# Performance work log

Hardware: AMD Instinct MI355X
Metric: run time of the kernel (lower is better)

Reference implementation:

```python
import jax, jax.numpy as jnp
import numpy as np
import math

D_MODEL, N_HEADS, BATCH, SEQ = 1024, 16, 2, 2048
D_HEAD = D_MODEL // N_HEADS


def setup_inputs() -> dict:
    key = jax.random.key(0)
    ks = jax.random.split(key, 5)
    w = lambda k: jax.random.normal(k, (D_MODEL, D_MODEL), jnp.float32) * 0.02
    return {
        "X": jax.random.normal(ks[0], (BATCH, SEQ, D_MODEL), jnp.float32),
        "W_q": w(ks[1]),
        "W_k": w(ks[2]),
        "W_v": w(ks[3]),
        "W_o": w(ks[4]),
        "g_q": jnp.ones((D_MODEL,), jnp.float32),
        "b_q": jnp.zeros((D_MODEL,), jnp.float32),
        "g_k": jnp.ones((D_MODEL,), jnp.float32),
        "b_k": jnp.zeros((D_MODEL,), jnp.float32),
        "cache_k": jnp.zeros((BATCH, N_HEADS, SEQ, D_HEAD), jnp.float32),
        "cache_v": jnp.zeros((BATCH, N_HEADS, SEQ, D_HEAD), jnp.float32),
        "start_pos": 0,
    }


def _layernorm(x, g, b, eps=1e-5):
    mu = jnp.mean(x, axis=-1, keepdims=True)
    xc = x - mu
    var = jnp.mean(xc * xc, axis=-1, keepdims=True)
    return xc * jax.lax.rsqrt(var + eps) * g + b


def reference(X, W_q, W_k, W_v, W_o, g_q, b_q, g_k, b_k, cache_k, cache_v, start_pos):
    batch, N, d_model = X.shape
    H = cache_k.shape[1]
    dh = d_model // H

    # QK-normed projections (torch Linear: x @ W^T)
    XQ = _layernorm(X @ W_q.T, g_q, b_q)
    XK = _layernorm(X @ W_k.T, g_k, b_k)
    XV = X @ W_v.T
    split = lambda t: t.reshape(batch, N, H, dh).transpose(0, 2, 1, 3)  # [b,h,n,d]
    XQ, XK, XV = split(XQ), split(XK), split(XV)

    # KV-cache scatter update, then slice to valid prefix (start_pos is static)
    cache_k = jax.lax.dynamic_update_slice(cache_k, XK, (0, 0, start_pos, 0))
    cache_v = jax.lax.dynamic_update_slice(cache_v, XV, (0, 0, start_pos, 0))
    M = start_pos + N
    K = cache_k[:, :, :M]
    V = cache_v[:, :, :M]

    logits = jnp.einsum('bhnd,bhmd->bhnm', XQ, K) / math.sqrt(dh)  # [b,h,N,M]

    # causal mask on the freshly written block [start_pos:M]
    tril = jnp.tril(jnp.ones((N, N), bool))
    full_mask = jnp.concatenate([jnp.ones((N, start_pos), bool), tril], axis=1)  # [N,M]
    logits = jnp.where(full_mask[None, None], logits, -jnp.inf)

    # selective forget-mask bias built from relu'd head-0 logits
    S = jax.nn.relu(logits[:, 0])               # relu(-inf) -> 0, matches torch
    S = S.at[..., 0].set(0.0)                   # zero first column
    S = S * (1.0 - jnp.eye(N, dtype=S.dtype))   # zero diagonal (valid since start_pos==0)
    S = jnp.roll(S, 1, axis=-2)                 # shift rows down by one
    S = S.at[..., 0, :].set(0.0)
    F_mask = jnp.cumsum(S, axis=-2)             # [b,N,M]

    logits = logits - F_mask[:, None]
    attn = jax.nn.softmax(logits, axis=-1)
    O = jnp.einsum('bhnm,bhmd->bhnd', attn, V)
    O = O.transpose(0, 2, 1, 3).reshape(batch, N, d_model)
    return O @ W_o.T
```

## Files before the change

kernel.cpp:

```cpp
#include <hip/hip_runtime.h>
#include <cstdint>
#include <cstddef>


typedef unsigned short u16;
typedef __attribute__((ext_vector_type(8))) __bf16 bf16x8;
typedef __attribute__((ext_vector_type(4))) float f32x4;
typedef __attribute__((ext_vector_type(2))) unsigned int uint2v;

#define D_MODEL 1024
#define N_HEADS 16
#define BATCH   2
#define SEQ     2048
#define D_HEAD  64
#define ROWS    (BATCH*SEQ)
#define NSEG    64
#define SEGLEN  32
#define LOG2E   1.44269504f

static __device__ __forceinline__ u16 f2bf(float f){
  union { float f; uint32_t u; } v; v.f = f;
  uint32_t r = v.u + 0x7fffu + ((v.u >> 16) & 1u);
  return (u16)(r >> 16);
}
static __device__ __forceinline__ float bf2f(u16 h){
  union { uint32_t u; float f; } v; v.u = ((uint32_t)h) << 16;
  return v.f;
}
static __device__ __forceinline__ uint32_t cvtpk(float lo, float hi){
  uint32_t r;
  asm("v_cvt_pk_bf16_f32 %0, %1, %2" : "=v"(r) : "v"(lo), "v"(hi));
  return r;
}
#define GLDS(gp, lp) __builtin_amdgcn_global_load_lds( \
    (const __attribute__((address_space(1))) void*)(gp), \
    (__attribute__((address_space(3))) void*)(lp), 16, 0, 0)

__global__ void k_cast_all(const float* __restrict__ X,
                           u16* __restrict__ Xhi, u16* __restrict__ Xlo,
                           const float* __restrict__ Wq,
                           u16* __restrict__ Wqh, u16* __restrict__ Wql,
                           const float* __restrict__ Wk,
                           u16* __restrict__ Wkh, u16* __restrict__ Wkl,
                           const float* __restrict__ Wv, u16* __restrict__ Wvb,
                           const float* __restrict__ Wo, u16* __restrict__ Wob){
  int i = blockIdx.x*256 + threadIdx.x;
  if (i < 1572864){
    const float* src; u16 *dh, *dl; int base;
    if (i < 1048576){ src = X;  dh = Xhi; dl = Xlo; base = i; }
    else if (i < 1310720){ src = Wq; dh = Wqh; dl = Wql; base = i - 1048576; }
    else { src = Wk; dh = Wkh; dl = Wkl; base = i - 1310720; }
    float4 v = reinterpret_cast<const float4*>(src)[base];
    float vs[4] = {v.x, v.y, v.z, v.w};
    union { u16 s[4]; uint2 u; } uh, ul;
#pragma unroll
    for (int r=0;r<4;++r){
      uh.s[r] = f2bf(vs[r]);
      ul.s[r] = f2bf(vs[r] - bf2f(uh.s[r]));
    }
    reinterpret_cast<uint2*>(dh)[base] = uh.u;
    reinterpret_cast<uint2*>(dl)[base] = ul.u;
  } else {
    const float* src; u16* dst; int base;
    if (i < 1835008){ src = Wv; dst = Wvb; base = i - 1572864; }
    else { src = Wo; dst = Wob; base = i - 1835008; }
    float4 v = reinterpret_cast<const float4*>(src)[base];
    float vs[4] = {v.x, v.y, v.z, v.w};
    union { u16 s[4]; uint2 u; } uh;
#pragma unroll
    for (int r=0;r<4;++r) uh.s[r] = f2bf(vs[r]);
    reinterpret_cast<uint2*>(dst)[base] = uh.u;
  }
}

__global__ __launch_bounds__(256) void k_mega(
    const u16* __restrict__ Xhi, const u16* __restrict__ Xlo,
    const u16* __restrict__ Wh,  const u16* __restrict__ Wl,
    const u16* __restrict__ Wvb,
    float* __restrict__ C, float* __restrict__ Dlt, u16* __restrict__ Vt)
{
  __shared__ __align__(16) u16 smem[16384];
  const int xj = blockIdx.x & 7, q = blockIdx.x >> 3;
  int section, idx;
  if (q < 64)      { section = 0; idx = xj*64 + q; }
  else if (q < 128){ section = 1; idx = xj*64 + (q-64); }
  else             { section = 2; idx = xj*16 + (q-128); }
  const int tid = threadIdx.x, wv = tid>>6, ln = tid&63;
  const int lane15 = ln&15, quad = ln>>4;
  const int wm = wv&1, wn = wv>>1;
  const int g = ln&7, sr = ln>>3;
  const int fs = lane15 & 7;
  f32x4 z = {0.f,0.f,0.f,0.f};
  u16* As = smem;
  u16* Bs = smem + 8192;

  if (section == 2){
    const int cx = idx & 1;
    const int cy = (idx >> 1) & 31;
    const int cz = idx >> 6;
    const size_t rowBase = (size_t)cy*128;
    const size_t wbase = cx ? (size_t)1024*1024 : 0;
    const u16* Ap = cz ? Xlo : Xhi;
    const u16* Bp = (cz ? Wh : Wl) + wbase;
    f32x4 acc[4][2];
#pragma unroll
    for (int i=0;i<4;++i){ acc[i][0] = z; acc[i][1] = z; }
    for (int kt = 0; kt < 16; ++kt) {
      __syncthreads();
#pragma unroll
      for (int c = 0; c < 4; ++c) {
        int chunk = wv*4 + c, r = chunk*8 + sr;
        GLDS(Ap + (rowBase + r)*1024 + kt*64 + (g^sr)*8, As + chunk*512);
      }
#pragma unroll
      for (int c = 0; c < 2; ++c) {
        int chunk = wv*2 + c, r = chunk*8 + sr;
        GLDS(Bp + (size_t)r*1024 + kt*64 + (g^sr)*8, Bs + chunk*512);
      }
      __syncthreads();
#pragma unroll
      for (int k2=0;k2<2;++k2){
        bf16x8 af[4], bfb[2];
#pragma unroll
        for (int t=0;t<4;++t)
          af[t]  = *reinterpret_cast<const bf16x8*>(As + (wm*64 + t*16 + lane15)*64 + (((k2*4+quad)^fs)*8));
#pragma unroll
        for (int t=0;t<2;++t)
          bfb[t] = *reinterpret_cast<const bf16x8*>(Bs + (wn*32 + t*16 + lane15)*64 + (((k2*4+quad)^fs)*8));
#pragma unroll
        for (int i=0;i<4;++i)
#pragma unroll
          for (int j=0;j<2;++j)
            acc[i][j] = __builtin_amdgcn_mfma_f32_16x16x32_bf16(af[i], bfb[j], acc[i][j], 0,0,0);
      }
    }
    float* Dp = Dlt + (size_t)cz*ROWS*128;
#pragma unroll
    for (int i=0;i<4;++i){
      size_t row = rowBase + wm*64 + i*16 + quad*4;
#pragma unroll
      for (int j=0;j<2;++j){
        size_t col = (size_t)cx*64 + wn*32 + j*16 + lane15;
#pragma unroll
        for (int r=0;r<4;++r)
          Dp[(row+r)*128 + col] = acc[i][j][r];
      }
    }
  } else if (section == 0){
    const size_t rowBase = (size_t)(idx>>4)*128, colBase = (size_t)(idx&15)*128;
    f32x4 acc[4][4];
#pragma unroll
    for (int i=0;i<4;++i)
#pragma unroll
      for (int j=0;j<4;++j) acc[i][j] = z;
    for (int kt = 0; kt < 16; ++kt) {
      __syncthreads();
#pragma unroll
      for (int c = 0; c < 4; ++c) {
        int chunk = wv*4 + c, r = chunk*8 + sr;
        GLDS(Xhi + (rowBase + r)*1024 + kt*64 + (g^sr)*8, As + chunk*512);
        GLDS(Wh  + (colBase + r)*1024 + kt*64 + (g^sr)*8, Bs + chunk*512);
      }
      __syncthreads();
#pragma unroll
      for (int k2=0;k2<2;++k2){
        bf16x8 af[4], bfb[4];
#pragma unroll
        for (int t=0;t<4;++t){
          af[t]  = *reinterpret_cast<const bf16x8*>(As + (wm*64 + t*16 + lane15)*64 + (((k2*4+quad)^fs)*8));
          bfb[t] = *reinterpret_cast<const bf16x8*>(Bs + (wn*64 + t*16 + lane15)*64 + (((k2*4+quad)^fs)*8));
        }
#pragma unroll
        for (int i=0;i<4;++i)
#pragma unroll
          for (int j=0;j<4;++j)
            acc[i][j] = __builtin_amdgcn_mfma_f32_16x16x32_bf16(af[i], bfb[j], acc[i][j], 0,0,0);
      }
    }
#pragma unroll
    for (int i=0;i<4;++i){
      size_t row = rowBase + wm*64 + i*16 + quad*4;
#pragma unroll
      for (int j=0;j<4;++j){
        size_t col = colBase + wn*64 + j*16 + lane15;
#pragma unroll
        for (int r=0;r<4;++r)
          C[(row+r)*2048 + col] = acc[i][j][r];
      }
    }
  } else {
    const int bx = idx & 15, by = idx >> 4;
    const size_t rowBase = (size_t)by*128, colBase = (size_t)bx*64;
    f32x4 acc[4][2];
#pragma unroll
    for (int i=0;i<4;++i){ acc[i][0] = z; acc[i][1] = z; }
    for (int kt = 0; kt < 16; ++kt) {
      __syncthreads();
#pragma unroll
      for (int c = 0; c < 4; ++c) {
        int chunk = wv*4 + c, r = chunk*8 + sr;
        GLDS(Xhi + (rowBase + r)*1024 + kt*64 + (g^sr)*8, As + chunk*512);
      }
#pragma unroll
      for (int c = 0; c < 2; ++c) {
        int chunk = wv*2 + c, r = chunk*8 + sr;
        GLDS(Wvb + (colBase + r)*1024 + kt*64 + (g^sr)*8, Bs + chunk*512);
      }
      __syncthreads();
#pragma unroll
      for (int k2=0;k2<2;++k2){
        bf16x8 af[4], bfb[2];
#pragma unroll
        for (int t=0;t<4;++t)
          af[t]  = *reinterpret_cast<const bf16x8*>(As + (wm*64 + t*16 + lane15)*64 + (((k2*4+quad)^fs)*8));
#pragma unroll
        for (int t=0;t<2;++t)
          bfb[t] = *reinterpret_cast<const bf16x8*>(Bs + (wn*32 + t*16 + lane15)*64 + (((k2*4+quad)^fs)*8));
#pragma unroll
        for (int i=0;i<4;++i)
#pragma unroll
          for (int j=0;j<2;++j)
            acc[i][j] = __builtin_amdgcn_mfma_f32_16x16x32_bf16(af[i], bfb[j], acc[i][j], 0,0,0);
      }
    }
    __syncthreads();
#pragma unroll
    for (int i=0;i<4;++i){
      int nl = wm*64 + i*16 + quad*4;
#pragma unroll
      for (int j=0;j<2;++j){
        int dl = wn*32 + j*16 + lane15;
#pragma unroll
        for (int r=0;r<4;++r)
          smem[dl*136 + nl + r] = f2bf(acc[i][j][r]);
      }
    }
    __syncthreads();
    const int b = by >> 4;
    const int n0 = (by & 15) * 128;
    const int bh = b*N_HEADS + bx;
    const int d = tid >> 2, seg = tid & 3;
    u16* dst = Vt + ((size_t)(bh*64 + d))*SEQ + n0 + seg*32;
    const u16* srcl = smem + d*136 + seg*32;
#pragma unroll
    for (int k=0;k<4;++k)
      *reinterpret_cast<uint4*>(dst + k*8) = *reinterpret_cast<const uint4*>(srcl + k*8);
  }
}

__global__ __launch_bounds__(256) void k_ln_pack2(
    const float* __restrict__ C, const float* __restrict__ Dlt,
    const float* __restrict__ gq, const float* __restrict__ bq,
    const float* __restrict__ gk, const float* __restrict__ bk,
    u16* __restrict__ Qh, u16* __restrict__ Kh,
    u16* __restrict__ Q0l, u16* __restrict__ K0l)
{
  const int row = blockIdx.x;
  const int tid = threadIdx.x;
  const float* cr = C + (size_t)row*2048;
  float4 vq = reinterpret_cast<const float4*>(cr)[tid];
  float4 vk = reinterpret_cast<const float4*>(cr)[256 + tid];
  const int h = tid >> 4;
  if (h == 0){
    const float* D0 = Dlt + (size_t)row*128;
    const float* D1 = Dlt + (size_t)ROWS*128 + (size_t)row*128;
    float4 a0 = reinterpret_cast<const float4*>(D0)[tid&15];
    float4 a1 = reinterpret_cast<const float4*>(D1)[tid&15];
    vq.x+=a0.x+a1.x; vq.y+=a0.y+a1.y; vq.z+=a0.z+a1.z; vq.w+=a0.w+a1.w;
    float4 b0 = reinterpret_cast<const float4*>(D0 + 64)[tid&15];
    float4 b1 = reinterpret_cast<const float4*>(D1 + 64)[tid&15];
    vk.x+=b0.x+b1.x; vk.y+=b0.y+b1.y; vk.z+=b0.z+b1.z; vk.w+=b0.w+b1.w;
  }
  float sq  = vq.x+vq.y+vq.z+vq.w;
  float s2q = vq.x*vq.x+vq.y*vq.y+vq.z*vq.z+vq.w*vq.w;
  float sk  = vk.x+vk.y+vk.z+vk.w;
  float s2k = vk.x*vk.x+vk.y*vk.y+vk.z*vk.z+vk.w*vk.w;
#pragma unroll
  for (int o=32;o;o>>=1){
    sq += __shfl_xor(sq,o);  s2q += __shfl_xor(s2q,o);
    sk += __shfl_xor(sk,o);  s2k += __shfl_xor(s2k,o);
  }
  __shared__ float red[4][4];
  if ((tid&63)==0){
    red[tid>>6][0]=sq; red[tid>>6][1]=s2q; red[tid>>6][2]=sk; red[tid>>6][3]=s2k;
  }
  __syncthreads();
  sq  = red[0][0]+red[1][0]+red[2][0]+red[3][0];
  s2q = red[0][1]+red[1][1]+red[2][1]+red[3][1];
  sk  = red[0][2]+red[1][2]+red[2][2]+red[3][2];
  s2k = red[0][3]+red[1][3]+red[2][3]+red[3][3];
  const float muq = sq*(1.f/D_MODEL);
  const float rsq = rsqrtf(s2q*(1.f/D_MODEL) - muq*muq + 1e-5f);
  const float muk = sk*(1.f/D_MODEL);
  const float rsk = rsqrtf(s2k*(1.f/D_MODEL) - muk*muk + 1e-5f);
  const int b = row >> 11, n = row & (SEQ-1);
  const int d0 = (tid & 15)*4;
  float4 gqv = reinterpret_cast<const float4*>(gq)[tid];
  float4 bqv = reinterpret_cast<const float4*>(bq)[tid];
  float4 gkv = reinterpret_cast<const float4*>(gk)[tid];
  float4 bkv = reinterpret_cast<const float4*>(bk)[tid];
  float xq[4] = {vq.x,vq.y,vq.z,vq.w}, xk[4] = {vk.x,vk.y,vk.z,vk.w};
  float gQ[4] = {gqv.x,gqv.y,gqv.z,gqv.w}, bQ[4] = {bqv.x,bqv.y,bqv.z,bqv.w};
  float gK[4] = {gkv.x,gkv.y,gkv.z,gkv.w}, bK[4] = {bkv.x,bkv.y,bkv.z,bkv.w};
  union { u16 s[4]; uint2 u; } qh, ql, kh, kl;
#pragma unroll
  for (int r=0;r<4;++r){
    float yq = (xq[r]-muq)*rsq*gQ[r] + bQ[r];
    qh.s[r] = f2bf(yq);
    ql.s[r] = f2bf(yq - bf2f(qh.s[r]));
    float yk = (xk[r]-muk)*rsk*gK[r] + bK[r];
    kh.s[r] = f2bf(yk);
    kl.s[r] = f2bf(yk - bf2f(kh.s[r]));
  }
  size_t dst = (((size_t)(b*N_HEADS + h))*SEQ + n)*D_HEAD + d0;
  *reinterpret_cast<uint2*>(Qh + dst) = qh.u;
  *reinterpret_cast<uint2*>(Kh + dst) = kh.u;
  if (h == 0){
    size_t dl = ((size_t)b*SEQ + n)*D_HEAD + d0;
    *reinterpret_cast<uint2*>(Q0l + dl) = ql.u;
    *reinterpret_cast<uint2*>(K0l + dl) = kl.u;
  }
}

__global__ __launch_bounds__(256) void k_s0(
    const u16* Qh, const u16* Q0l, const u16* Kh, const u16* K0l,
    float* __restrict__ S0, float* __restrict__ seg)
{
  const int b = blockIdx.z;
  const int bm = blockIdx.y;
  const int bn = blockIdx.x;
  const int tid = threadIdx.x;
  if (bn > bm){
    for (int t = tid; t < 512; t += 256)
      seg[((size_t)b*NSEG + bm*4 + (t>>7))*SEQ + bn*128 + (t&127)] = 0.f;
    return;
  }
  float* Sb = S0 + (size_t)b*SEQ*SEQ;
  __shared__ __align__(16) u16 smem[4*8192];
  const int wv = tid>>6, ln = tid&63;
  const int lane15 = ln&15, quad = ln>>4;
  const int wm = wv&1, wn = wv>>1;
  const int g = ln&7, sr = ln>>3;
  const int fs = lane15 & 7;
  const size_t rowBase = (size_t)bm*128, colBase = (size_t)bn*128;
  const u16* srcs[4] = {
    Qh  + ((size_t)b*N_HEADS*SEQ + rowBase)*D_HEAD,
    Q0l + ((size_t)b*SEQ + rowBase)*D_HEAD,
    Kh  + ((size_t)b*N_HEADS*SEQ + colBase)*D_HEAD,
    K0l + ((size_t)b*SEQ + colBase)*D_HEAD };
#pragma unroll
  for (int t=0;t<4;++t){
#pragma unroll
    for (int c=0;c<4;++c){
      int chunk = wv*4 + c, r = chunk*8 + sr;
      GLDS(srcs[t] + (size_t)r*64 + (g^sr)*8, smem + t*8192 + chunk*512);
    }
  }
  __syncthreads();
  f32x4 acc[4][4];
  f32x4 z = {0.f,0.f,0.f,0.f};
#pragma unroll
  for (int i=0;i<4;++i)
#pragma unroll
    for (int j=0;j<4;++j) acc[i][j] = z;
  const int Aidx[3] = {0, 0, 1};
  const int Bidx[3] = {2, 3, 2};
#pragma unroll
  for (int p = 0; p < 3; ++p){
    const u16* At = smem + Aidx[p]*8192;
    const u16* Bt = smem + Bidx[p]*8192;
#pragma unroll
    for (int k2=0;k2<2;++k2){
      bf16x8 af[4], bfb[4];
#pragma unroll
      for (int t=0;t<4;++t){
        af[t]  = *reinterpret_cast<const bf16x8*>(At + (wm*64 + t*16 + lane15)*64 + (((k2*4+quad)^fs)*8));
        bfb[t] = *reinterpret_cast<const bf16x8*>(Bt + (wn*64 + t*16 + lane15)*64 + (((k2*4+quad)^fs)*8));
      }
#pragma unroll
      for (int i=0;i<4;++i)
#pragma unroll
        for (int j=0;j<4;++j)
          acc[i][j] = __builtin_amdgcn_mfma_f32_16x16x32_bf16(af[i], bfb[j], acc[i][j], 0,0,0);
    }
  }
  float csum[2][4] = {{0.f,0.f,0.f,0.f},{0.f,0.f,0.f,0.f}};
#pragma unroll
  for (int i=0;i<4;++i){
#pragma unroll
    for (int j=0;j<4;++j){
#pragma unroll
      for (int r=0;r<4;++r){
        int jg = (int)rowBase + wm*64 + i*16 + quad*4 + r;
        int mg = (int)colBase + wn*64 + j*16 + lane15;
        float l = acc[i][j][r]*0.125f;
        float s = (mg >= 1 && mg < jg) ? fmaxf(l, 0.f) : 0.f;
        Sb[(size_t)jg*SEQ + mg] = s;
        csum[i>>1][j] += s;
      }
    }
  }
  __syncthreads();
  float* cs = (float*)smem;
#pragma unroll
  for (int h2=0;h2<2;++h2){
#pragma unroll
    for (int j=0;j<4;++j){
      float v = csum[h2][j];
      v += __shfl_xor(v, 16);
      v += __shfl_xor(v, 32);
      if (ln < 16) cs[(wm*2 + h2)*128 + wn*64 + j*16 + ln] = v;
    }
  }
  __syncthreads();
  for (int t = tid; t < 512; t += 256)
    seg[((size_t)b*NSEG + bm*4 + (t>>7))*SEQ + bn*128 + (t&127)] = cs[t];
}

__global__ void k_segpfx(float* __restrict__ seg){
  const int gidx = blockIdx.x*256 + threadIdx.x;
  const int b = gidx >> 11, m = gidx & (SEQ-1);
  float* col = seg + (size_t)b*NSEG*SEQ + m;
  float run = 0.f;
#pragma unroll
  for (int s=0; s<NSEG; ++s){
    float v = col[(size_t)s*SEQ];
    col[(size_t)s*SEQ] = run;
    run += v;
  }
}

__global__ void k_seg_apply(float* __restrict__ SF, const float* __restrict__ seg){
  int m = blockIdx.x*256 + threadIdx.x;
  int s = blockIdx.y, b = blockIdx.z;
  float run = seg[((size_t)b*NSEG + s)*SEQ + m];
  float* Sb = SF + (size_t)b*SEQ*SEQ;
  const int j0 = s*SEGLEN;
#pragma unroll 8
  for (int i=0;i<SEGLEN;++i){
    size_t idx = (size_t)(j0 + i)*SEQ + m;
    float t = Sb[idx];
    Sb[idx] = -run*LOG2E;
    run += (j0 + i > m) ? t : 0.f;
  }
}

__constant__ unsigned char WMAP[48] = {
  62,63,60,79,
  61,58,59,56,78,
  57,54,55,52,77,
  53,50,51,48,76,
  49,46,47,44,75,
  45,42,43,40,74,
  41,38,39,36,73,
  37,34,35,32,72,
  33,71,
  70,69,68,67,66,65,64};

__global__ __launch_bounds__(256, 4) void k_attn(
    const u16* __restrict__ Qh, const u16* __restrict__ Kh,
    const u16* __restrict__ Vt, const float* __restrict__ F,
    u16* __restrict__ Ob, float* __restrict__ Opart, float* __restrict__ Ps)
{
  __shared__ __align__(16) u16 Ks[2][64*64];
  __shared__ __align__(16) u16 Vs[2][64*64];
  const int w = blockIdx.x;
  const int bh = w & 31, b = bh >> 4, h = bh & 15;
  const int item = (int)WMAP[w >> 5];
  int nt, mt0, mt1, segi;
  if (item >= 64){ nt = item - 64; segi = 0; mt0 = 0; mt1 = nt; }
  else {
    nt = item >> 1; segi = item & 1;
    const int half = (nt + 2) >> 1;
    mt0 = segi ? half : 0;
    mt1 = segi ? nt : (half - 1);
  }
  const bool partial = (item < 64);
  const int tid = threadIdx.x, wv = tid>>6, ln = tid&63;
  const int lane15 = ln&15, quad = ln>>4;
  const u16* Qbh = Qh + ((size_t)(b*N_HEADS + h))*SEQ*D_HEAD;
  const u16* Kbh = Kh + ((size_t)(b*N_HEADS + h))*SEQ*D_HEAD;
  const u16* Vbh = Vt + ((size_t)(b*N_HEADS + h))*D_HEAD*SEQ;
  const int n_loc = wv*16 + lane15;
  const int n_g = nt*64 + n_loc;
  const float* Frow = F + (size_t)b*SEQ*SEQ + (size_t)n_g*SEQ;
  const int swz = (ln&7) ^ ((ln>>3)&7);
  const int fswz = lane15 & 7;
  const int srow = ln>>3;

  bf16x8 qf[2];
#pragma unroll
  for (int kt=0; kt<2; ++kt)
    qf[kt] = *reinterpret_cast<const bf16x8*>(Qbh + (size_t)n_g*D_HEAD + kt*32 + quad*8);

  f32x4 z = {0.f,0.f,0.f,0.f};
  f32x4 psum = z;
  f32x4 acc_o[4];
#pragma unroll
  for (int no=0;no<4;++no) acc_o[no] = z;

  auto stage = [&](int mt, int buf){
#pragma unroll
    for (int c=0;c<2;++c){
      int chunk = wv*2 + c;
      int r = chunk*8 + srow;
      GLDS(Kbh + (size_t)(mt*64 + r)*D_HEAD + swz*8, &Ks[buf][chunk*512]);
      GLDS(Vbh + (size_t)r*SEQ + mt*64 + swz*8,      &Vs[buf][chunk*512]);
    }
  };
  stage(mt0, mt0 & 1);
  f32x4 fvn[4];
#pragma unroll
  for (int ms=0; ms<4; ++ms)
    fvn[ms] = *reinterpret_cast<const f32x4*>(Frow + mt0*64 + ms*16 + quad*4);
  const float c1 = 0.125f*LOG2E;

  for (int mt = mt0; mt <= mt1; ++mt) {
    const int cur = mt & 1;
    __syncthreads();
    if (mt < mt1) stage(mt+1, 1-cur);
    f32x4 fv[4];
#pragma unroll
    for (int ms=0; ms<4; ++ms) fv[ms] = fvn[ms];
    if (mt < mt1){
      const float* Fr1 = Frow + (mt+1)*64;
#pragma unroll
      for (int ms=0; ms<4; ++ms)
        fvn[ms] = *reinterpret_cast<const f32x4*>(Fr1 + ms*16 + quad*4);
    }
    f32x4 accs[4];
    __builtin_amdgcn_s_setprio(1);
#pragma unroll
    for (int ms=0; ms<4; ++ms){
      bf16x8 a = *reinterpret_cast<const bf16x8*>(
          &Ks[cur][(ms*16 + lane15)*64 + ((quad ^ fswz) * 8)]);
      accs[ms] = __builtin_amdgcn_mfma_f32_16x16x32_bf16(a, qf[0], z, 0,0,0);
    }
#pragma unroll
    for (int ms=0; ms<4; ++ms){
      bf16x8 a = *reinterpret_cast<const bf16x8*>(
          &Ks[cur][(ms*16 + lane15)*64 + (((4 + quad) ^ fswz) * 8)]);
      accs[ms] = __builtin_amdgcn_mfma_f32_16x16x32_bf16(a, qf[1], accs[ms], 0,0,0);
    }
    __builtin_amdgcn_s_setprio(0);
    uint32_t pw[4][2];
    if (mt == nt){
#pragma unroll
      for (int ms=0; ms<4; ++ms){
        const int ml = ms*16 + quad*4;
        float l0 = fmaf(accs[ms][0], c1, fv[ms][0]);
        float l1 = fmaf(accs[ms][1], c1, fv[ms][1]);
        float l2 = fmaf(accs[ms][2], c1, fv[ms][2]);
        float l3 = fmaf(accs[ms][3], c1, fv[ms][3]);
        if (ml + 0 > n_loc) l0 = -1e30f;
        if (ml + 1 > n_loc) l1 = -1e30f;
        if (ml + 2 > n_loc) l2 = -1e30f;
        if (ml + 3 > n_loc) l3 = -1e30f;
        float p0 = __builtin_amdgcn_exp2f(l0);
        float p1 = __builtin_amdgcn_exp2f(l1);
        float p2 = __builtin_amdgcn_exp2f(l2);
        float p3 = __builtin_amdgcn_exp2f(l3);
        psum[0]+=p0; psum[1]+=p1; psum[2]+=p2; psum[3]+=p3;
        pw[ms][0] = cvtpk(p0, p1);
        pw[ms][1] = cvtpk(p2, p3);
      }
    } else {
#pragma unroll
      for (int ms=0; ms<4; ++ms){
        float p0 = __builtin_amdgcn_exp2f(fmaf(accs[ms][0], c1, fv[ms][0]));
        float p1 = __builtin_amdgcn_exp2f(fmaf(accs[ms][1], c1, fv[ms][1]));
        float p2 = __builtin_amdgcn_exp2f(fmaf(accs[ms][2], c1, fv[ms][2]));
        float p3 = __builtin_amdgcn_exp2f(fmaf(accs[ms][3], c1, fv[ms][3]));
        psum[0]+=p0; psum[1]+=p1; psum[2]+=p2; psum[3]+=p3;
        pw[ms][0] = cvtpk(p0, p1);
        pw[ms][1] = cvtpk(p2, p3);
      }
    }
    __builtin_amdgcn_s_setprio(1);
#pragma unroll
    for (int kt=0; kt<2; ++kt){
      union { uint32_t u[4]; bf16x8 v; } pa;
#pragma unroll
      for (int pr=0; pr<2; ++pr){
        uint2v s32 = __builtin_amdgcn_permlane32_swap(
            pw[2*kt][pr], pw[2*kt+1][pr], false, false);
        uint2v s16 = __builtin_amdgcn_permlane16_swap(s32.x, s32.y, false, false);
        pa.u[pr]   = s16.x;
        pa.u[2+pr] = s16.y;
      }
#pragma unroll
      for (int no=0; no<4; ++no){
        int d = no*16 + lane15;
        bf16x8 vb = *reinterpret_cast<const bf16x8*>(
            &Vs[cur][d*64 + (((kt*4 + quad) ^ (d&7)) * 8)]);
        acc_o[no] = __builtin_amdgcn_mfma_f32_16x16x32_bf16(pa.v, vb, acc_o[no], 0,0,0);
      }
    }
    __builtin_amdgcn_s_setprio(0);
  }
  float s = (psum[0]+psum[1]) + (psum[2]+psum[3]);
  s += __shfl_xor(s, 16);
  s += __shfl_xor(s, 32);
  if (partial){
    const size_t pb = (size_t)(bh*16 + (nt - 16))*2 + segi;
    float* Op = Opart + pb*4096;
    if (quad == 0) Ps[pb*64 + wv*16 + lane15] = s;
#pragma unroll
    for (int no=0; no<4; ++no)
#pragma unroll
      for (int r=0;r<4;++r)
        Op[(wv*16 + quad*4 + r)*64 + no*16 + lane15] = acc_o[no][r];
  } else {
    f32x4 inv;
#pragma unroll
    for (int r=0;r<4;++r)
      inv[r] = __builtin_amdgcn_rcpf(__shfl(s, quad*4 + r));
#pragma unroll
    for (int no=0; no<4; ++no){
#pragma unroll
      for (int r=0;r<4;++r){
        float o = acc_o[no][r] * inv[r];
        int row = nt*64 + wv*16 + quad*4 + r;
        Ob[((size_t)(b*SEQ + row))*D_MODEL + h*64 + no*16 + lane15] = f2bf(o);
      }
    }
  }
}

__global__ __launch_bounds__(256) void k_comb(
    const float* __restrict__ Opart, const float* __restrict__ Ps,
    u16* __restrict__ Ob)
{
  const int t = blockIdx.x;
  const int bh = t >> 4, b = bh >> 4, h = bh & 15;
  const int nt = (t & 15) + 16;
  const int tid = threadIdx.x;
  const int row = tid >> 2, c0 = (tid & 3) * 16;
  const float* P0 = Opart + (size_t)t*2*4096 + row*64 + c0;
  const float* P1 = P0 + 4096;
  const float s = Ps[(size_t)t*128 + row] + Ps[(size_t)t*128 + 64 + row];
  const float inv = __builtin_amdgcn_rcpf(s);
  union { u16 us[16]; uint4 u[2]; } o;
#pragma unroll
  for (int g2=0; g2<4; ++g2){
    float4 a = reinterpret_cast<const float4*>(P0)[g2];
    float4 c = reinterpret_cast<const float4*>(P1)[g2];
    o.us[g2*4+0] = f2bf((a.x + c.x) * inv);
    o.us[g2*4+1] = f2bf((a.y + c.y) * inv);
    o.us[g2*4+2] = f2bf((a.z + c.z) * inv);
    o.us[g2*4+3] = f2bf((a.w + c.w) * inv);
  }
  u16* dst = Ob + ((size_t)(b*SEQ + nt*64 + row))*D_MODEL + h*64 + c0;
  reinterpret_cast<uint4*>(dst)[0] = o.u[0];
  reinterpret_cast<uint4*>(dst)[1] = o.u[1];
}

__global__ __launch_bounds__(256) void k_gemm_nt64(
    const u16* __restrict__ A0, const u16* __restrict__ B0,
    float* __restrict__ C, int N, int K)
{
  __shared__ __align__(16) u16 As[8192];
  __shared__ __align__(16) u16 Bs[4096];
  const int tid = threadIdx.x, wv = tid>>6, ln = tid&63;
  const int lane15 = ln&15, quad = ln>>4;
  const int wm = wv&1, wn = wv>>1;
  const int g = ln&7, sr = ln>>3;
  const int fs = lane15 & 7;
  const size_t rowBase = (size_t)blockIdx.y*128, colBase = (size_t)blockIdx.x*64;
  f32x4 acc[4][2];
  f32x4 z = {0.f,0.f,0.f,0.f};
#pragma unroll
  for (int i=0;i<4;++i){ acc[i][0] = z; acc[i][1] = z; }
  const int ktiles = K >> 6;
  for (int kt = 0; kt < ktiles; ++kt) {
    __syncthreads();
#pragma unroll
    for (int c = 0; c < 4; ++c) {
      int chunk = wv*4 + c, r = chunk*8 + sr;
      GLDS(A0 + (rowBase + r)*K + kt*64 + (g^sr)*8, As + chunk*512);
    }
#pragma unroll
    for (int c = 0; c < 2; ++c) {
      int chunk = wv*2 + c, r = chunk*8 + sr;
      GLDS(B0 + (colBase + r)*K + kt*64 + (g^sr)*8, Bs + chunk*512);
    }
    __syncthreads();
#pragma unroll
    for (int k2=0;k2<2;++k2){
      bf16x8 af[4], bfb[2];
#pragma unroll
      for (int t=0;t<4;++t)
        af[t]  = *reinterpret_cast<const bf16x8*>(As + (wm*64 + t*16 + lane15)*64 + (((k2*4+quad)^fs)*8));
#pragma unroll
      for (int t=0;t<2;++t)
        bfb[t] = *reinterpret_cast<const bf16x8*>(Bs + (wn*32 + t*16 + lane15)*64 + (((k2*4+quad)^fs)*8));
#pragma unroll
      for (int i=0;i<4;++i)
#pragma unroll
        for (int j=0;j<2;++j)
          acc[i][j] = __builtin_amdgcn_mfma_f32_16x16x32_bf16(af[i], bfb[j], acc[i][j], 0,0,0);
    }
  }
#pragma unroll
  for (int i=0;i<4;++i){
    size_t row = rowBase + wm*64 + i*16 + quad*4;
#pragma unroll
    for (int j=0;j<2;++j){
      size_t col = colBase + wn*32 + j*16 + lane15;
#pragma unroll
      for (int r=0;r<4;++r)
        C[(row+r)*N + col] = acc[i][j][r];
    }
  }
}

extern "C" void kernel_launch(void* const* d_in, const int* in_sizes, int n_in,
                              void* d_out, int out_size, void* d_ws, size_t ws_size,
                              hipStream_t stream)
{
  (void)in_sizes; (void)n_in; (void)out_size; (void)ws_size;
  const float* X  = (const float*)d_in[0];
  const float* Wq = (const float*)d_in[1];
  const float* Wk = (const float*)d_in[2];
  const float* Wv = (const float*)d_in[3];
  const float* Wo = (const float*)d_in[4];
  const float* gq = (const float*)d_in[5];
  const float* bq = (const float*)d_in[6];
  const float* gk = (const float*)d_in[7];
  const float* bk = (const float*)d_in[8];
  float* out = (float*)d_out;

  char* ws = (char*)d_ws;
  size_t off = 0;
  auto alloc = [&](size_t bytes)->char*{
    char* p = ws + off; off += (bytes + 255) & ~(size_t)255; return p;
  };
  u16* Xhi  = (u16*)alloc((size_t)ROWS*D_MODEL*2);
  u16* Xlo  = (u16*)alloc((size_t)ROWS*D_MODEL*2);
  u16* Wqkh = (u16*)alloc((size_t)2*D_MODEL*D_MODEL*2);
  u16* Wqkl = (u16*)alloc((size_t)2*D_MODEL*D_MODEL*2);
  u16* Wvb  = (u16*)alloc((size_t)D_MODEL*D_MODEL*2);
  u16* Wob  = (u16*)alloc((size_t)D_MODEL*D_MODEL*2);
  u16* Qhp  = (u16*)alloc((size_t)BATCH*N_HEADS*SEQ*D_HEAD*2);
  u16* Khp  = (u16*)alloc((size_t)BATCH*N_HEADS*SEQ*D_HEAD*2);
  u16* Q0l  = (u16*)alloc((size_t)BATCH*SEQ*D_HEAD*2);
  u16* K0l  = (u16*)alloc((size_t)BATCH*SEQ*D_HEAD*2);
  u16* Vtp  = (u16*)alloc((size_t)BATCH*N_HEADS*D_HEAD*SEQ*2);
  u16* Obf  = (u16*)alloc((size_t)ROWS*D_MODEL*2);
  float* Dlt = (float*)alloc((size_t)2*ROWS*128*4);
  float* Seg = (float*)alloc((size_t)BATCH*NSEG*SEQ*4);
  float* Opart = (float*)alloc((size_t)512*2*4096*4);
  float* Ps    = (float*)alloc((size_t)512*2*64*4);
  float* SF  = (float*)alloc((size_t)BATCH*SEQ*SEQ*4);
  float* C32 = SF;

  k_cast_all<<<8192, 256, 0, stream>>>(
      X, Xhi, Xlo,
      Wq, Wqkh, Wqkl,
      Wk, Wqkh + (size_t)D_MODEL*D_MODEL, Wqkl + (size_t)D_MODEL*D_MODEL,
      Wv, Wvb, Wo, Wob);
  k_mega<<<1152, 256, 0, stream>>>(Xhi, Xlo, Wqkh, Wqkl, Wvb, C32, Dlt, Vtp);
  k_ln_pack2<<<ROWS, 256, 0, stream>>>(C32, Dlt, gq, bq, gk, bk, Qhp, Khp, Q0l, K0l);
  k_s0<<<dim3(16, 16, BATCH), 256, 0, stream>>>(Qhp, Q0l, Khp, K0l, SF, Seg);
  k_segpfx<<<16, 256, 0, stream>>>(Seg);
  k_seg_apply<<<dim3(8, NSEG, BATCH), 256, 0, stream>>>(SF, Seg);
  k_attn<<<1536, 256, 0, stream>>>(Qhp, Khp, Vtp, SF, Obf, Opart, Ps);
  k_comb<<<512, 256, 0, stream>>>(Opart, Ps, Obf);
  k_gemm_nt64<<<dim3(16, 32), 256, 0, stream>>>(Obf, Wob, out, D_MODEL, D_MODEL);
}
```

Measured before the change: 277.2 us.

## Split attention blocks into single-wave blocks reading K/V directly from global

The attention kernel drops its shared-memory double-buffered K/V staging and barriers. Each block is now a single wave that loads K and V fragments straight from global memory into registers. To make those loads contiguous, the V-transpose writer stores V in 64x64 chunk-major tiles. This removes LDS traffic and block-wide syncs, but each wave now fetches K/V separately (four times the global/L2 reads), and the software prefetch of the next F tile and K/V is gone.

```diff
diff --git a/kernel.cpp b/kernel.cpp
--- a/kernel.cpp
+++ b/kernel.cpp
@@ -237,10 +237,10 @@
     }
     __syncthreads();
     const int b = by >> 4;
-    const int n0 = (by & 15) * 128;
     const int bh = b*N_HEADS + bx;
     const int d = tid >> 2, seg = tid & 3;
-    u16* dst = Vt + ((size_t)(bh*64 + d))*SEQ + n0 + seg*32;
+    const int chunk = (by & 15)*2 + (seg >> 1);
+    u16* dst = Vt + ((size_t)(bh*32 + chunk)*64 + d)*64 + (seg & 1)*32;
     const u16* srcl = smem + d*136 + seg*32;
 #pragma unroll
     for (int k=0;k<4;++k)
@@ -457,16 +457,15 @@
   33,71,
   70,69,68,67,66,65,64};
 
-__global__ __launch_bounds__(256, 4) void k_attn(
+__global__ __launch_bounds__(64, 4) void k_attn(
     const u16* __restrict__ Qh, const u16* __restrict__ Kh,
     const u16* __restrict__ Vt, const float* __restrict__ F,
     u16* __restrict__ Ob, float* __restrict__ Opart, float* __restrict__ Ps)
 {
-  __shared__ __align__(16) u16 Ks[2][64*64];
-  __shared__ __align__(16) u16 Vs[2][64*64];
   const int w = blockIdx.x;
-  const int bh = w & 31, b = bh >> 4, h = bh & 15;
-  const int item = (int)WMAP[w >> 5];
+  const int wv = w & 3;
+  const int bh = (w >> 2) & 31, b = bh >> 4, h = bh & 15;
+  const int item = (int)WMAP[w >> 7];
   int nt, mt0, mt1, segi;
   if (item >= 64){ nt = item - 64; segi = 0; mt0 = 0; mt1 = nt; }
   else {
@@ -476,17 +475,15 @@
     mt1 = segi ? nt : (half - 1);
   }
   const bool partial = (item < 64);
-  const int tid = threadIdx.x, wv = tid>>6, ln = tid&63;
+  const int ln = threadIdx.x & 63;
   const int lane15 = ln&15, quad = ln>>4;
   const u16* Qbh = Qh + ((size_t)(b*N_HEADS + h))*SEQ*D_HEAD;
   const u16* Kbh = Kh + ((size_t)(b*N_HEADS + h))*SEQ*D_HEAD;
-  const u16* Vbh = Vt + ((size_t)(b*N_HEADS + h))*D_HEAD*SEQ;
+  const u16* Vbh = Vt + ((size_t)(b*N_HEADS + h))*SEQ*D_HEAD;
   const int n_loc = wv*16 + lane15;
   const int n_g = nt*64 + n_loc;
   const float* Frow = F + (size_t)b*SEQ*SEQ + (size_t)n_g*SEQ;
-  const int swz = (ln&7) ^ ((ln>>3)&7);
-  const int fswz = lane15 & 7;
-  const int srow = ln>>3;
+  const float c1 = 0.125f*LOG2E;
 
   bf16x8 qf[2];
 #pragma unroll
@@ -499,50 +496,34 @@
 #pragma unroll
   for (int no=0;no<4;++no) acc_o[no] = z;
 
-  auto stage = [&](int mt, int buf){
-#pragma unroll
-    for (int c=0;c<2;++c){
-      int chunk = wv*2 + c;
-      int r = chunk*8 + srow;
-      GLDS(Kbh + (size_t)(mt*64 + r)*D_HEAD + swz*8, &Ks[buf][chunk*512]);
-      GLDS(Vbh + (size_t)r*SEQ + mt*64 + swz*8,      &Vs[buf][chunk*512]);
-    }
-  };
-  stage(mt0, mt0 & 1);
-  f32x4 fvn[4];
-#pragma unroll
-  for (int ms=0; ms<4; ++ms)
-    fvn[ms] = *reinterpret_cast<const f32x4*>(Frow + mt0*64 + ms*16 + quad*4);
-  const float c1 = 0.125f*LOG2E;
-
   for (int mt = mt0; mt <= mt1; ++mt) {
-    const int cur = mt & 1;
-    __syncthreads();
-    if (mt < mt1) stage(mt+1, 1-cur);
+    const u16* Kc = Kbh + (size_t)mt*64*D_HEAD;
+    const u16* Vc = Vbh + (size_t)mt*64*D_HEAD;
+    bf16x8 kf0[4], kf1[4];
+#pragma unroll
+    for (int ms=0; ms<4; ++ms){
+      kf0[ms] = *reinterpret_cast<const bf16x8*>(Kc + (ms*16 + lane15)*64 + quad*8);
+      kf1[ms] = *reinterpret_cast<const bf16x8*>(Kc + (ms*16 + lane15)*64 + 32 + quad*8);
+    }
     f32x4 fv[4];
 #pragma unroll
-    for (int ms=0; ms<4; ++ms) fv[ms] = fvn[ms];
-    if (mt < mt1){
-      const float* Fr1 = Frow + (mt+1)*64;
-#pragma unroll
-      for (int ms=0; ms<4; ++ms)
-        fvn[ms] = *reinterpret_cast<const f32x4*>(Fr1 + ms*16 + quad*4);
-    }
+    for (int ms=0; ms<4; ++ms)
+      fv[ms] = *reinterpret_cast<const f32x4*>(Frow + mt*64 + ms*16 + quad*4);
     f32x4 accs[4];
     __builtin_amdgcn_s_setprio(1);
 #pragma unroll
-    for (int ms=0; ms<4; ++ms){
-      bf16x8 a = *reinterpret_cast<const bf16x8*>(
-          &Ks[cur][(ms*16 + lane15)*64 + ((quad ^ fswz) * 8)]);
-      accs[ms] = __builtin_amdgcn_mfma_f32_16x16x32_bf16(a, qf[0], z, 0,0,0);
-    }
-#pragma unroll
-    for (int ms=0; ms<4; ++ms){
-      bf16x8 a = *reinterpret_cast<const bf16x8*>(
-          &Ks[cur][(ms*16 + lane15)*64 + (((4 + quad) ^ fswz) * 8)]);
-      accs[ms] = __builtin_amdgcn_mfma_f32_16x16x32_bf16(a, qf[1], accs[ms], 0,0,0);
-    }
+    for (int ms=0; ms<4; ++ms)
+      accs[ms] = __builtin_amdgcn_mfma_f32_16x16x32_bf16(kf0[ms], qf[0], z, 0,0,0);
+#pragma unroll
+    for (int ms=0; ms<4; ++ms)
+      accs[ms] = __builtin_amdgcn_mfma_f32_16x16x32_bf16(kf1[ms], qf[1], accs[ms], 0,0,0);
     __builtin_amdgcn_s_setprio(0);
+    bf16x8 vf0[4], vf1[4];
+#pragma unroll
+    for (int no=0; no<4; ++no){
+      vf0[no] = *reinterpret_cast<const bf16x8*>(Vc + (no*16 + lane15)*64 + quad*8);
+      vf1[no] = *reinterpret_cast<const bf16x8*>(Vc + (no*16 + lane15)*64 + 32 + quad*8);
+    }
     uint32_t pw[4][2];
     if (mt == nt){
 #pragma unroll
@@ -590,9 +571,7 @@
       }
 #pragma unroll
       for (int no=0; no<4; ++no){
-        int d = no*16 + lane15;
-        bf16x8 vb = *reinterpret_cast<const bf16x8*>(
-            &Vs[cur][d*64 + (((kt*4 + quad) ^ (d&7)) * 8)]);
+        bf16x8 vb = kt ? vf1[no] : vf0[no];
         acc_o[no] = __builtin_amdgcn_mfma_f32_16x16x32_bf16(pa.v, vb, acc_o[no], 0,0,0);
       }
     }
@@ -764,7 +743,7 @@
   k_s0<<<dim3(16, 16, BATCH), 256, 0, stream>>>(Qhp, Q0l, Khp, K0l, SF, Seg);
   k_segpfx<<<16, 256, 0, stream>>>(Seg);
   k_seg_apply<<<dim3(8, NSEG, BATCH), 256, 0, stream>>>(SF, Seg);
-  k_attn<<<1536, 256, 0, stream>>>(Qhp, Khp, Vtp, SF, Obf, Opart, Ps);
+  k_attn<<<6144, 64, 0, stream>>>(Qhp, Khp, Vtp, SF, Obf, Opart, Ps);
   k_comb<<<512, 256, 0, stream>>>(Opart, Ps, Obf);
   k_gemm_nt64<<<dim3(16, 32), 256, 0, stream>>>(Obf, Wob, out, D_MODEL, D_MODEL);
 }
```

Result: slower. 381.1 us (+37.4%).

## Split causal attention rows into up to four fixed 8-tile KV segments

Applied to the files above, without the earlier changes.

Attention work is now partitioned into KV segments of at most eight 64-wide tiles. Query tiles 8 to 31 are split into two, three or four partial work items instead of the previous two-way split of tiles 16 to 31. A new 80-entry schedule orders the items longest-first. The combine kernel now sums a variable number of partial outputs and softmax denominators. The aim is better load balance and more parallel blocks for long causal rows, at the cost of more partial-output traffic and a heavier combine step.

```diff
diff --git a/kernel.cpp b/kernel.cpp
--- a/kernel.cpp
+++ b/kernel.cpp
@@ -445,17 +445,22 @@
   }
 }
 
-__constant__ unsigned char WMAP[48] = {
-  62,63,60,79,
-  61,58,59,56,78,
-  57,54,55,52,77,
-  53,50,51,48,76,
-  49,46,47,44,75,
-  45,42,43,40,74,
-  41,38,39,36,73,
-  37,34,35,32,72,
-  33,71,
-  70,69,68,67,66,65,64};
+__constant__ unsigned char WMAP80[80] = {
+  124,125,126,127,
+  120,121,122,  116,117,118,  112,113,114,  108,109,110,
+  104,105,106,  100,101,102,   96, 97, 98,
+   92, 93, 94,
+   88, 89,  84, 85,  80, 81,  76, 77,  72, 73,  68, 69,  64, 65,
+   60, 61,
+   56, 52, 48, 44, 40, 36, 32,
+   28,
+  123, 90, 57, 24,
+  119, 86, 53, 20,
+  115, 82, 49, 16,
+  111, 78, 45, 12,
+  107, 74, 41,  8,
+  103, 70, 37,  4,
+   99, 66, 33,  0};
 
 __global__ __launch_bounds__(256, 4) void k_attn(
     const u16* __restrict__ Qh, const u16* __restrict__ Kh,
@@ -466,16 +471,11 @@
   __shared__ __align__(16) u16 Vs[2][64*64];
   const int w = blockIdx.x;
   const int bh = w & 31, b = bh >> 4, h = bh & 15;
-  const int item = (int)WMAP[w >> 5];
-  int nt, mt0, mt1, segi;
-  if (item >= 64){ nt = item - 64; segi = 0; mt0 = 0; mt1 = nt; }
-  else {
-    nt = item >> 1; segi = item & 1;
-    const int half = (nt + 2) >> 1;
-    mt0 = segi ? half : 0;
-    mt1 = segi ? nt : (half - 1);
-  }
-  const bool partial = (item < 64);
+  const int item = (int)WMAP80[w >> 5];
+  const int nt = item >> 2, segi = item & 3;
+  const int mt0 = segi * 8;
+  const int mt1 = (nt < mt0 + 7) ? nt : (mt0 + 7);
+  const bool partial = (nt >= 8);
   const int tid = threadIdx.x, wv = tid>>6, ln = tid&63;
   const int lane15 = ln&15, quad = ln>>4;
   const u16* Qbh = Qh + ((size_t)(b*N_HEADS + h))*SEQ*D_HEAD;
@@ -602,7 +602,10 @@
   s += __shfl_xor(s, 16);
   s += __shfl_xor(s, 32);
   if (partial){
-    const size_t pb = (size_t)(bh*16 + (nt - 16))*2 + segi;
+    const int base = (nt < 16) ? (nt-8)*2
+                   : (nt < 24) ? 16 + (nt-16)*3
+                               : 40 + (nt-24)*4;
+    const size_t pb = (size_t)(bh*72 + base + segi);
     float* Op = Opart + pb*4096;
     if (quad == 0) Ps[pb*64 + wv*16 + lane15] = s;
 #pragma unroll
@@ -632,24 +635,34 @@
     u16* __restrict__ Ob)
 {
   const int t = blockIdx.x;
-  const int bh = t >> 4, b = bh >> 4, h = bh & 15;
-  const int nt = (t & 15) + 16;
+  const int bh = t / 24, tloc = t % 24;
+  const int b = bh >> 4, h = bh & 15;
+  const int nt = 8 + tloc;
+  const int nseg = (tloc < 8) ? 2 : (tloc < 16) ? 3 : 4;
+  const int base = (tloc < 8) ? tloc*2
+                 : (tloc < 16) ? 16 + (tloc-8)*3
+                               : 40 + (tloc-16)*4;
+  const size_t slot0 = (size_t)bh*72 + base;
   const int tid = threadIdx.x;
   const int row = tid >> 2, c0 = (tid & 3) * 16;
-  const float* P0 = Opart + (size_t)t*2*4096 + row*64 + c0;
-  const float* P1 = P0 + 4096;
-  const float s = Ps[(size_t)t*128 + row] + Ps[(size_t)t*128 + 64 + row];
+  float s = 0.f;
+  for (int g2 = 0; g2 < nseg; ++g2) s += Ps[(slot0 + g2)*64 + row];
   const float inv = __builtin_amdgcn_rcpf(s);
+  float acc[16];
+#pragma unroll
+  for (int e=0;e<16;++e) acc[e] = 0.f;
+  for (int g2 = 0; g2 < nseg; ++g2){
+    const float* P = Opart + (slot0 + g2)*4096 + row*64 + c0;
+#pragma unroll
+    for (int q4=0; q4<4; ++q4){
+      float4 a = reinterpret_cast<const float4*>(P)[q4];
+      acc[q4*4+0] += a.x; acc[q4*4+1] += a.y;
+      acc[q4*4+2] += a.z; acc[q4*4+3] += a.w;
+    }
+  }
   union { u16 us[16]; uint4 u[2]; } o;
 #pragma unroll
-  for (int g2=0; g2<4; ++g2){
-    float4 a = reinterpret_cast<const float4*>(P0)[g2];
-    float4 c = reinterpret_cast<const float4*>(P1)[g2];
-    o.us[g2*4+0] = f2bf((a.x + c.x) * inv);
-    o.us[g2*4+1] = f2bf((a.y + c.y) * inv);
-    o.us[g2*4+2] = f2bf((a.z + c.z) * inv);
-    o.us[g2*4+3] = f2bf((a.w + c.w) * inv);
-  }
+  for (int e=0;e<16;++e) o.us[e] = f2bf(acc[e] * inv);
   u16* dst = Ob + ((size_t)(b*SEQ + nt*64 + row))*D_MODEL + h*64 + c0;
   reinterpret_cast<uint4*>(dst)[0] = o.u[0];
   reinterpret_cast<uint4*>(dst)[1] = o.u[1];
@@ -749,8 +762,8 @@
   u16* Obf  = (u16*)alloc((size_t)ROWS*D_MODEL*2);
   float* Dlt = (float*)alloc((size_t)2*ROWS*128*4);
   float* Seg = (float*)alloc((size_t)BATCH*NSEG*SEQ*4);
-  float* Opart = (float*)alloc((size_t)512*2*4096*4);
-  float* Ps    = (float*)alloc((size_t)512*2*64*4);
+  float* Opart = (float*)alloc((size_t)32*72*4096*4);
+  float* Ps    = (float*)alloc((size_t)32*72*64*4);
   float* SF  = (float*)alloc((size_t)BATCH*SEQ*SEQ*4);
   float* C32 = SF;
 
@@ -764,7 +777,7 @@
   k_s0<<<dim3(16, 16, BATCH), 256, 0, stream>>>(Qhp, Q0l, Khp, K0l, SF, Seg);
   k_segpfx<<<16, 256, 0, stream>>>(Seg);
   k_seg_apply<<<dim3(8, NSEG, BATCH), 256, 0, stream>>>(SF, Seg);
-  k_attn<<<1536, 256, 0, stream>>>(Qhp, Khp, Vtp, SF, Obf, Opart, Ps);
-  k_comb<<<512, 256, 0, stream>>>(Opart, Ps, Obf);
+  k_attn<<<2560, 256, 0, stream>>>(Qhp, Khp, Vtp, SF, Obf, Opart, Ps);
+  k_comb<<<768, 256, 0, stream>>>(Opart, Ps, Obf);
   k_gemm_nt64<<<dim3(16, 32), 256, 0, stream>>>(Obf, Wob, out, D_MODEL, D_MODEL);
 }
```

New measurement: 279.7 us. Within noise of the previous version (+0.9%).
